# Kernel tuning notes

Hardware: AMD Instinct MI355X
Metric: run time of the kernel (lower is better)

The kernel has to match this reference:

```python
import jax, jax.numpy as jnp
import numpy as np
import math

N_HEAD = 16

def _rope_tables(seq, dh, dtype):
    inv_freq = 1.0 / (10000.0 ** (jnp.arange(0, dh, 2, dtype=jnp.float32) / dh))
    angle = jnp.arange(seq, dtype=jnp.float32)[:, None] * inv_freq[None, :]  # [S, dh/2]
    sin = jnp.repeat(jnp.sin(angle), 2, axis=-1).astype(dtype)  # [S, dh]
    cos = jnp.repeat(jnp.cos(angle), 2, axis=-1).astype(dtype)
    return sin, cos

def _rotate_half(x):
    x_even = x[..., ::2]
    x_odd = x[..., 1::2]
    return jnp.stack([-x_odd, x_even], axis=-1).reshape(x.shape)

def _apply_rope(x, sin, cos):
    # x: [B, H, S, dh]; sin/cos: [S, dh]
    return x * cos[None, None] + _rotate_half(x) * sin[None, None]

def setup_inputs() -> dict:
    key = jax.random.key(0)
    ks = jax.random.split(key, 9)
    B, S, D = 2, 2048, 2048
    scale = 1.0 / math.sqrt(D)
    x = jax.random.normal(ks[0], (B, S, D), dtype=jnp.float32)
    wq = jax.random.normal(ks[1], (D, D), dtype=jnp.float32) * scale
    wk = jax.random.normal(ks[2], (D, D), dtype=jnp.float32) * scale
    wv = jax.random.normal(ks[3], (D, D), dtype=jnp.float32) * scale
    wo = jax.random.normal(ks[4], (D, D), dtype=jnp.float32) * scale
    bq = jnp.zeros((D,), jnp.float32)
    bk = jnp.zeros((D,), jnp.float32)
    bv = jnp.zeros((D,), jnp.float32)
    bo = jnp.zeros((D,), jnp.float32)
    # causal mask: True = masked (strict upper triangle)
    mask = jnp.triu(jnp.ones((S, S), dtype=bool), k=1)[None, None]  # [1,1,S,S]
    return {"x": x, "wq": wq, "bq": bq, "wk": wk, "bk": bk, "wv": wv, "bv": bv,
            "wo": wo, "bo": bo, "mask": mask}

def reference(x, wq, bq, wk, bk, wv, bv, wo, bo, mask):
    B, S, D = x.shape
    H = N_HEAD
    dh = D // H
    # projections (torch Linear: x @ W.T + b)
    q = (x @ wq.T + bq).reshape(B, S, H, dh).transpose(0, 2, 1, 3)  # [B,H,S,dh]
    k = (x @ wk.T + bk).reshape(B, S, H, dh).transpose(0, 2, 1, 3)
    v = (x @ wv.T + bv).reshape(B, S, H, dh).transpose(0, 2, 1, 3)
    sin, cos = _rope_tables(S, dh, x.dtype)
    q = _apply_rope(q, sin, cos)
    k = _apply_rope(k, sin, cos)
    scores = jnp.einsum('bhqd,bhkd->bhqk', q, k) / math.sqrt(dh)
    scores = jnp.where(mask, -jnp.inf, scores)
    attn = jax.nn.softmax(scores, axis=-1)
    attn = jnp.nan_to_num(attn, nan=0.0)
    out = jnp.einsum('bhqk,bhkd->bhqd', attn, v)  # [B,H,S,dh]
    out = out.transpose(0, 2, 1, 3).reshape(B, S, D)
    return out @ wo.T + bo
```

## Files before the change

### kernel.cpp

```cpp
#include <hip/hip_runtime.h>
#include <math.h>


typedef _Float16 half8 __attribute__((ext_vector_type(8)));
typedef _Float16 half4v __attribute__((ext_vector_type(4)));
typedef float f32x4 __attribute__((ext_vector_type(4)));

__device__ __forceinline__ void gl_lds16(const void* g, void* l) {
  __builtin_amdgcn_global_load_lds(
      (const __attribute__((address_space(1))) unsigned int*)g,
      (__attribute__((address_space(3))) unsigned int*)l, 16, 0, 0);
}

__global__ void cast_f32_f16(const float* __restrict__ src, _Float16* __restrict__ dst, int n4) {
  int i = blockIdx.x * blockDim.x + threadIdx.x;
  if (i >= n4) return;
  float4 v = reinterpret_cast<const float4*>(src)[i];
  half4v o;
  o[0] = (_Float16)v.x; o[1] = (_Float16)v.y; o[2] = (_Float16)v.z; o[3] = (_Float16)v.w;
  reinterpret_cast<half4v*>(dst)[i] = o;
}

__global__ void cast_w(const float* __restrict__ w0, const float* __restrict__ w1,
                       const float* __restrict__ w2, const float* __restrict__ w3,
                       _Float16* __restrict__ wdst) {
  const float* s = blockIdx.y == 0 ? w0 : blockIdx.y == 1 ? w1 : blockIdx.y == 2 ? w2 : w3;
  int i = blockIdx.x * blockDim.x + threadIdx.x;
  float4 v = reinterpret_cast<const float4*>(s)[i];
  half4v o;
  o[0] = (_Float16)v.x; o[1] = (_Float16)v.y; o[2] = (_Float16)v.z; o[3] = (_Float16)v.w;
  reinterpret_cast<half4v*>(wdst)[(size_t)blockIdx.y * 1048576 + i] = o;
}

template <bool OUT_F32>
__global__ __launch_bounds__(512, 2) void gemm_bt256(
    const _Float16* __restrict__ A,
    const _Float16* __restrict__ B,
    const float* __restrict__ b0, const float* __restrict__ b1,
    const float* __restrict__ b2,
    void* __restrict__ Cout,
    int M, int N, int K) {
  __shared__ _Float16 As[2][16384];
  __shared__ _Float16 Bs[2][16384];
  const int bm = blockIdx.y * 256, bn = blockIdx.x * 256;
  const int tid = threadIdx.x;
  const int wave = tid >> 6, lane = tid & 63;
  const int quad = lane >> 4, l16 = lane & 15;
  const int wm = (wave >> 2) * 128, wn = (wave & 3) * 64;

  const int srow = tid >> 3;
  const int sx = (tid & 7) ^ (srow & 7);
  const _Float16* Ag = A + (size_t)(bm + srow) * K + sx * 8;
  const _Float16* Bg[4];
#pragma unroll
  for (int c = 0; c < 4; ++c) {
    int r = (((c * 2 + (srow >> 5)) & 3) << 6) + ((c >> 1) << 5) + (srow & 31);
    Bg[c] = B + (size_t)(bn + r) * K + sx * 8;
  }

#define STAGE_A(buf, R, kt) \
  gl_lds16(Ag + (size_t)(R) * K + (kt) * 64, &As[buf][(R) * 64 + tid * 8])
#define STAGE_B(buf, c, kt) \
  gl_lds16(Bg[c] + (kt) * 64, &Bs[buf][(c) * 4096 + tid * 8])

  const int axor = l16 & 7;
  const int sl0 = ((0 + quad) ^ axor) * 8;
  const int sl1 = ((4 + quad) ^ axor) * 8;
  const int aoff = (wm + l16) * 64;
  const int q4 = (wn >> 6) * 32;

#define RD_A(i, kk) \
  (*reinterpret_cast<const half8*>(&As[cur][aoff + (i) * 1024 + ((kk) ? sl1 : sl0)]))
#define RD_B(j, kk) \
  (*reinterpret_cast<const half8*>( \
      &Bs[cur][((((j) >> 1) * 128 + q4 + ((j) & 1) * 16 + l16)) * 64 + ((kk) ? sl1 : sl0)]))

  f32x4 acc[8][4];
#pragma unroll
  for (int i = 0; i < 8; ++i)
#pragma unroll
    for (int j = 0; j < 4; ++j) acc[i][j] = f32x4{0.f, 0.f, 0.f, 0.f};

  half8 a[4][2], b[4][2];
  const int NT = K >> 6;

  STAGE_A(0, 0, 0); STAGE_A(0, 128, 0);
  STAGE_B(0, 0, 0); STAGE_B(0, 1, 0);
  STAGE_B(0, 2, 0); STAGE_B(0, 3, 0);
  STAGE_A(0, 64, 0); STAGE_A(0, 192, 0);
  if (NT > 1) {
    STAGE_A(1, 0, 1); STAGE_A(1, 128, 1);
    STAGE_B(1, 0, 1); STAGE_B(1, 1, 1);
    STAGE_B(1, 2, 1); STAGE_B(1, 3, 1);
    asm volatile("s_waitcnt vmcnt(6)");
  } else {
    asm volatile("s_waitcnt vmcnt(0)");
  }
  __builtin_amdgcn_s_barrier();

  for (int t = 0; t < NT; ++t) {
    const int cur = t & 1, nxt = cur ^ 1;
    const bool pf1 = (t + 1 < NT);
    const bool pf2 = (t + 2 < NT);

#pragma unroll
    for (int i = 0; i < 4; ++i) {
      a[i][0] = RD_A(i, 0); a[i][1] = RD_A(i, 1);
    }
#pragma unroll
    for (int j = 0; j < 2; ++j) {
      b[j][0] = RD_B(j, 0); b[j][1] = RD_B(j, 1);
    }
    if (pf1) { STAGE_A(nxt, 64, t + 1); STAGE_A(nxt, 192, t + 1); }
    __builtin_amdgcn_s_barrier();
    __builtin_amdgcn_s_setprio(1);
#pragma unroll
    for (int i = 0; i < 4; ++i)
#pragma unroll
      for (int j = 0; j < 2; ++j) {
        acc[i][j] = __builtin_amdgcn_mfma_f32_16x16x32_f16(a[i][0], b[j][0], acc[i][j], 0, 0, 0);
        acc[i][j] = __builtin_amdgcn_mfma_f32_16x16x32_f16(a[i][1], b[j][1], acc[i][j], 0, 0, 0);
      }
    __builtin_amdgcn_s_setprio(0);
    __builtin_amdgcn_s_barrier();

#pragma unroll
    for (int j = 2; j < 4; ++j) {
      b[j][0] = RD_B(j, 0); b[j][1] = RD_B(j, 1);
    }
    if (pf2) { STAGE_A(cur, 0, t + 2); STAGE_A(cur, 128, t + 2); }
    __builtin_amdgcn_s_barrier();
    __builtin_amdgcn_s_setprio(1);
#pragma unroll
    for (int i = 0; i < 4; ++i)
#pragma unroll
      for (int j = 2; j < 4; ++j) {
        acc[i][j] = __builtin_amdgcn_mfma_f32_16x16x32_f16(a[i][0], b[j][0], acc[i][j], 0, 0, 0);
        acc[i][j] = __builtin_amdgcn_mfma_f32_16x16x32_f16(a[i][1], b[j][1], acc[i][j], 0, 0, 0);
      }
    __builtin_amdgcn_s_setprio(0);
    __builtin_amdgcn_s_barrier();

#pragma unroll
    for (int i = 0; i < 4; ++i) {
      a[i][0] = RD_A(i + 4, 0); a[i][1] = RD_A(i + 4, 1);
    }
    if (pf2) { STAGE_B(cur, 0, t + 2); STAGE_B(cur, 1, t + 2); }
    __builtin_amdgcn_s_barrier();
    __builtin_amdgcn_s_setprio(1);
#pragma unroll
    for (int i = 0; i < 4; ++i)
#pragma unroll
      for (int j = 0; j < 2; ++j) {
        acc[i + 4][j] = __builtin_amdgcn_mfma_f32_16x16x32_f16(a[i][0], b[j][0], acc[i + 4][j], 0, 0, 0);
        acc[i + 4][j] = __builtin_amdgcn_mfma_f32_16x16x32_f16(a[i][1], b[j][1], acc[i + 4][j], 0, 0, 0);
      }
    __builtin_amdgcn_s_setprio(0);
    __builtin_amdgcn_s_barrier();

    if (pf2) { STAGE_B(cur, 2, t + 2); STAGE_B(cur, 3, t + 2); }
    __builtin_amdgcn_s_barrier();
    __builtin_amdgcn_s_setprio(1);
#pragma unroll
    for (int i = 0; i < 4; ++i)
#pragma unroll
      for (int j = 2; j < 4; ++j) {
        acc[i + 4][j] = __builtin_amdgcn_mfma_f32_16x16x32_f16(a[i][0], b[j][0], acc[i + 4][j], 0, 0, 0);
        acc[i + 4][j] = __builtin_amdgcn_mfma_f32_16x16x32_f16(a[i][1], b[j][1], acc[i + 4][j], 0, 0, 0);
      }
    __builtin_amdgcn_s_setprio(0);
    if (pf2)
      asm volatile("s_waitcnt vmcnt(6)");
    else
      asm volatile("s_waitcnt vmcnt(0)");
    __builtin_amdgcn_s_barrier();
  }

#pragma unroll
  for (int j = 0; j < 4; ++j) {
    const int gc = bn + wn + j * 16 + l16;
    const float* bp = (gc < 2048) ? b0 : (gc < 4096 ? b1 : b2);
    const float bz = bp[gc & 2047];
#pragma unroll
    for (int i = 0; i < 8; ++i) {
#pragma unroll
      for (int r = 0; r < 4; ++r) {
        const int gr = bm + wm + i * 16 + quad * 4 + r;
        float v = acc[i][j][r] + bz;
        if (OUT_F32)
          reinterpret_cast<float*>(Cout)[(size_t)gr * N + gc] = v;
        else
          reinterpret_cast<_Float16*>(Cout)[(size_t)gr * N + gc] = (_Float16)v;
      }
    }
  }
#undef STAGE_A
#undef STAGE_B
#undef RD_A
#undef RD_B
}

__global__ void rope_inplace(_Float16* __restrict__ qkv, int ngroups) {
  int idx = blockIdx.x * blockDim.x + threadIdx.x;
  if (idx >= ngroups) return;
  int m = idx >> 8;
  int g = idx & 255;
  int s = m & 2047;
  const float scale = 0.088388347648318447f;
  size_t base = (size_t)m * 6144 + g * 8;
  half8 qv = *reinterpret_cast<const half8*>(qkv + base);
  half8 kv = *reinterpret_cast<const half8*>(qkv + base + 2048);
  half8 qo, ko;
#pragma unroll
  for (int j = 0; j < 4; ++j) {
    int i = (g * 4 + j) & 63;
    float ang = (float)s * exp2f(-0.2076205059304601f * (float)i);
    float sn, cs;
    __sincosf(ang, &sn, &cs);
    float e = (float)qv[j * 2], o = (float)qv[j * 2 + 1];
    qo[j * 2]     = (_Float16)((e * cs - o * sn) * scale);
    qo[j * 2 + 1] = (_Float16)((o * cs + e * sn) * scale);
    e = (float)kv[j * 2]; o = (float)kv[j * 2 + 1];
    ko[j * 2]     = (_Float16)(e * cs - o * sn);
    ko[j * 2 + 1] = (_Float16)(o * cs + e * sn);
  }
  *reinterpret_cast<half8*>(qkv + base) = qo;
  *reinterpret_cast<half8*>(qkv + base + 2048) = ko;
}

__global__ __launch_bounds__(256) void transpose_v(const _Float16* __restrict__ qkv,
                                                   _Float16* __restrict__ vt) {
  __shared__ _Float16 t[64][72];
  const int s0 = blockIdx.x * 64;
  const int d0 = blockIdx.y * 64;
  const int bh = blockIdx.z;
  const int b = bh >> 4, h = bh & 15;
  const int tid = threadIdx.x;
#pragma unroll
  for (int p = 0; p < 2; ++p) {
    int chunk = p * 256 + tid;
    int r = chunk >> 3, c8 = (chunk & 7) * 8;
    *reinterpret_cast<half8*>(&t[r][c8]) = *reinterpret_cast<const half8*>(
        &qkv[(size_t)(b * 2048 + s0 + r) * 6144 + 4096 + h * 128 + d0 + c8]);
  }
  __syncthreads();
#pragma unroll
  for (int p = 0; p < 2; ++p) {
    int chunk = p * 256 + tid;
    int dr = chunk >> 3, c8 = (chunk & 7) * 8;
    half8 o;
#pragma unroll
    for (int j = 0; j < 8; ++j) o[j] = t[c8 + j][dr];
    *reinterpret_cast<half8*>(&vt[(size_t)(bh * 128 + d0 + dr) * 2048 + s0 + c8]) = o;
  }
}

__global__ __launch_bounds__(256, 2) void attn_kernel(
    const _Float16* __restrict__ QKV,
    const _Float16* __restrict__ VT,
    _Float16* __restrict__ ctx) {
  constexpr int LD = 6144, S = 2048;
  __shared__ _Float16 Ks[2][8192];
  __shared__ _Float16 Vs[2][8192];
  __shared__ _Float16 P[4][16][80];
  const int bid = blockIdx.x;
  const int bh = bid & 31;
  const int qt = 31 - (bid >> 5);
  const int b = bh >> 4, h = bh & 15;
  const int tid = threadIdx.x;
  const int wv = tid >> 6, lane = tid & 63;
  const int quad = lane >> 4, l16 = lane & 15;
  const int q0 = qt * 64 + wv * 16;

  const _Float16* qp = QKV + (size_t)(b * S + q0 + l16) * LD + h * 128;
  half8 aq[4];
#pragma unroll
  for (int ks = 0; ks < 4; ++ks)
    aq[ks] = *reinterpret_cast<const half8*>(qp + ks * 32 + quad * 8);

  const _Float16* gk[4];
  const _Float16* gv[4];
  int lofs[4];
#pragma unroll
  for (int p = 0; p < 4; ++p) {
    int c = p * 256 + tid;
    int cs = c ^ ((c >> 3) & 7);
    int cl16 = cs & 15, cqd = (cs >> 4) & 3;
    int cks = (cs >> 6) & 3, cf = cs >> 8;
    gk[p] = QKV + (size_t)(b * S + cf * 16 + cl16) * LD + 2048 + h * 128 + cks * 32 + cqd * 8;
    int ckv = (cs >> 6) & 1, ct = cs >> 7;
    gv[p] = VT + (size_t)(bh * 128 + ct * 16 + cl16) * S + ckv * 32 + cqd * 8;
    lofs[p] = c * 8;
  }

  const int kofs = (l16 >> 3) * 64 + (((l16 & 7) ^ (quad * 2 + (l16 >> 3)))) * 8;

  f32x4 acc[8];
#pragma unroll
  for (int t = 0; t < 8; ++t) acc[t] = f32x4{0.f, 0.f, 0.f, 0.f};
  f32x4 lacc = f32x4{0.f, 0.f, 0.f, 0.f};

  half8 ones;
#pragma unroll
  for (int j = 0; j < 8; ++j) ones[j] = (_Float16)1.0f;

#pragma unroll
  for (int p = 0; p < 4; ++p) gl_lds16(gk[p], &Ks[0][lofs[p]]);
#pragma unroll
  for (int p = 0; p < 4; ++p) gl_lds16(gv[p], &Vs[0][lofs[p]]);

  for (int j = 0; j <= qt; ++j) {
    __syncthreads();
    const int cur = j & 1;
    if (j < qt) {
      const size_t ko = (size_t)(j + 1) * 64 * LD;
      const int vo = (j + 1) * 64;
#pragma unroll
      for (int p = 0; p < 4; ++p) gl_lds16(gk[p] + ko, &Ks[cur ^ 1][lofs[p]]);
#pragma unroll
      for (int p = 0; p < 4; ++p) gl_lds16(gv[p] + vo, &Vs[cur ^ 1][lofs[p]]);
    }
    f32x4 sf[4];
#pragma unroll
    for (int f = 0; f < 4; ++f) sf[f] = f32x4{0.f, 0.f, 0.f, 0.f};
#pragma unroll
    for (int f = 0; f < 4; ++f)
#pragma unroll
      for (int ks = 0; ks < 4; ++ks) {
        half8 bk = *reinterpret_cast<const half8*>(&Ks[cur][((f * 4 + ks) * 4 + quad) * 128 + kofs]);
        sf[f] = __builtin_amdgcn_mfma_f32_16x16x32_f16(aq[ks], bk, sf[f], 0, 0, 0);
      }
    if (j == qt) {
      const int key0 = j * 64;
#pragma unroll
      for (int f = 0; f < 4; ++f) {
        const int key = key0 + f * 16 + l16;
#pragma unroll
        for (int r = 0; r < 4; ++r) {
          const int row = q0 + quad * 4 + r;
          sf[f][r] = (key <= row) ? sf[f][r] : -1e30f;
        }
      }
    }
#pragma unroll
    for (int f = 0; f < 4; ++f)
#pragma unroll
      for (int r = 0; r < 4; ++r)
        P[wv][quad * 4 + r][f * 16 + l16] = (_Float16)__expf(sf[f][r] - 5.0f);
    half8 pa0 = *reinterpret_cast<const half8*>(&P[wv][l16][quad * 8]);
    half8 pa1 = *reinterpret_cast<const half8*>(&P[wv][l16][32 + quad * 8]);
#pragma unroll
    for (int t = 0; t < 8; ++t) {
      half8 bv0 = *reinterpret_cast<const half8*>(&Vs[cur][((t * 2 + 0) * 4 + quad) * 128 + kofs]);
      half8 bv1 = *reinterpret_cast<const half8*>(&Vs[cur][((t * 2 + 1) * 4 + quad) * 128 + kofs]);
      acc[t] = __builtin_amdgcn_mfma_f32_16x16x32_f16(pa0, bv0, acc[t], 0, 0, 0);
      acc[t] = __builtin_amdgcn_mfma_f32_16x16x32_f16(pa1, bv1, acc[t], 0, 0, 0);
    }
    lacc = __builtin_amdgcn_mfma_f32_16x16x32_f16(pa0, ones, lacc, 0, 0, 0);
    lacc = __builtin_amdgcn_mfma_f32_16x16x32_f16(pa1, ones, lacc, 0, 0, 0);
  }

  float inv[4];
#pragma unroll
  for (int r = 0; r < 4; ++r) inv[r] = 1.0f / lacc[r];
#pragma unroll
  for (int t = 0; t < 8; ++t)
#pragma unroll
    for (int r = 0; r < 4; ++r)
      ctx[(size_t)(b * S + q0 + quad * 4 + r) * 2048 + h * 128 + t * 16 + l16] =
          (_Float16)(acc[t][r] * inv[r]);
}

extern "C" void kernel_launch(void* const* d_in, const int* in_sizes, int n_in,
                              void* d_out, int out_size, void* d_ws, size_t ws_size,
                              hipStream_t stream) {
  const float* x  = (const float*)d_in[0];
  const float* wq = (const float*)d_in[1];
  const float* bq = (const float*)d_in[2];
  const float* wk = (const float*)d_in[3];
  const float* bk = (const float*)d_in[4];
  const float* wv = (const float*)d_in[5];
  const float* bv = (const float*)d_in[6];
  const float* wo = (const float*)d_in[7];
  const float* bo = (const float*)d_in[8];

  _Float16* W      = (_Float16*)d_ws;
  _Float16* xh     = W;
  _Float16* wqkvh  = xh + 8388608;
  _Float16* woh    = wqkvh + 12582912;
  _Float16* qkvlin = woh + 4194304;
  _Float16* vT     = xh;
  _Float16* ctx    = wqkvh;

  cast_f32_f16<<<8192, 256, 0, stream>>>(x, xh, 2097152);
  cast_w<<<dim3(4096, 4), 256, 0, stream>>>(wq, wk, wv, wo, wqkvh);

  gemm_bt256<false><<<dim3(24, 16), 512, 0, stream>>>(xh, wqkvh, bq, bk, bv, qkvlin,
                                                      4096, 6144, 2048);

  rope_inplace<<<4096, 256, 0, stream>>>(qkvlin, 1048576);
  transpose_v<<<dim3(32, 2, 32), 256, 0, stream>>>(qkvlin, vT);
  attn_kernel<<<1024, 256, 0, stream>>>(qkvlin, vT, ctx);

  gemm_bt256<true><<<dim3(8, 16), 512, 0, stream>>>(ctx, woh, bo, bo, bo, (float*)d_out,
                                                    4096, 2048, 2048);
}
```

Before: 439.5 us.

## Process two query tiles per attention block to reuse K/V loads

Each attention block now handles 128 query rows, split into two 64-row halves, and shares every K/V tile loaded into LDS between both halves. This halves the grid and the global-to-LDS traffic per query. It also orders blocks so that heavy and light causal tiles interleave. The cost is roughly twice the accumulator registers per thread, which may lower occupancy under the existing launch bounds, plus extra branching on the last tile.

```diff
diff --git a/kernel.cpp b/kernel.cpp
--- a/kernel.cpp
+++ b/kernel.cpp
@@ -265,18 +265,22 @@
   __shared__ _Float16 P[4][16][80];
   const int bid = blockIdx.x;
   const int bh = bid & 31;
-  const int qt = 31 - (bid >> 5);
+  const int idx = (bid >> 5) & 7;
+  const int qb = (bid >> 8) ? idx : 15 - idx;
   const int b = bh >> 4, h = bh & 15;
   const int tid = threadIdx.x;
   const int wv = tid >> 6, lane = tid & 63;
   const int quad = lane >> 4, l16 = lane & 15;
-  const int q0 = qt * 64 + wv * 16;
-
-  const _Float16* qp = QKV + (size_t)(b * S + q0 + l16) * LD + h * 128;
-  half8 aq[4];
-#pragma unroll
-  for (int ks = 0; ks < 4; ++ks)
-    aq[ks] = *reinterpret_cast<const half8*>(qp + ks * 32 + quad * 8);
+  const int q0 = qb * 128 + wv * 16;
+  const int NJ = 2 * qb + 2;
+
+  const _Float16* qp0 = QKV + (size_t)(b * S + q0 + l16) * LD + h * 128;
+  half8 aq0[4], aq1[4];
+#pragma unroll
+  for (int ks = 0; ks < 4; ++ks) {
+    aq0[ks] = *reinterpret_cast<const half8*>(qp0 + ks * 32 + quad * 8);
+    aq1[ks] = *reinterpret_cast<const half8*>(qp0 + (size_t)64 * LD + ks * 32 + quad * 8);
+  }
 
   const _Float16* gk[4];
   const _Float16* gv[4];
@@ -295,10 +299,14 @@
 
   const int kofs = (l16 >> 3) * 64 + (((l16 & 7) ^ (quad * 2 + (l16 >> 3)))) * 8;
 
-  f32x4 acc[8];
-#pragma unroll
-  for (int t = 0; t < 8; ++t) acc[t] = f32x4{0.f, 0.f, 0.f, 0.f};
-  f32x4 lacc = f32x4{0.f, 0.f, 0.f, 0.f};
+  f32x4 acc0[8], acc1[8];
+#pragma unroll
+  for (int t = 0; t < 8; ++t) {
+    acc0[t] = f32x4{0.f, 0.f, 0.f, 0.f};
+    acc1[t] = f32x4{0.f, 0.f, 0.f, 0.f};
+  }
+  f32x4 lacc0 = f32x4{0.f, 0.f, 0.f, 0.f};
+  f32x4 lacc1 = f32x4{0.f, 0.f, 0.f, 0.f};
 
   half8 ones;
 #pragma unroll
@@ -309,10 +317,10 @@
 #pragma unroll
   for (int p = 0; p < 4; ++p) gl_lds16(gv[p], &Vs[0][lofs[p]]);
 
-  for (int j = 0; j <= qt; ++j) {
+  for (int j = 0; j < NJ; ++j) {
     __syncthreads();
     const int cur = j & 1;
-    if (j < qt) {
+    if (j + 1 < NJ) {
       const size_t ko = (size_t)(j + 1) * 64 * LD;
       const int vo = (j + 1) * 64;
 #pragma unroll
@@ -320,55 +328,91 @@
 #pragma unroll
       for (int p = 0; p < 4; ++p) gl_lds16(gv[p] + vo, &Vs[cur ^ 1][lofs[p]]);
     }
-    f32x4 sf[4];
-#pragma unroll
-    for (int f = 0; f < 4; ++f) sf[f] = f32x4{0.f, 0.f, 0.f, 0.f};
+    const bool h0 = (j < NJ - 1);
+    f32x4 sf0[4], sf1[4];
+#pragma unroll
+    for (int f = 0; f < 4; ++f) {
+      sf0[f] = f32x4{0.f, 0.f, 0.f, 0.f};
+      sf1[f] = f32x4{0.f, 0.f, 0.f, 0.f};
+    }
 #pragma unroll
     for (int f = 0; f < 4; ++f)
 #pragma unroll
       for (int ks = 0; ks < 4; ++ks) {
         half8 bk = *reinterpret_cast<const half8*>(&Ks[cur][((f * 4 + ks) * 4 + quad) * 128 + kofs]);
-        sf[f] = __builtin_amdgcn_mfma_f32_16x16x32_f16(aq[ks], bk, sf[f], 0, 0, 0);
-      }
-    if (j == qt) {
-      const int key0 = j * 64;
+        sf0[f] = __builtin_amdgcn_mfma_f32_16x16x32_f16(aq0[ks], bk, sf0[f], 0, 0, 0);
+        sf1[f] = __builtin_amdgcn_mfma_f32_16x16x32_f16(aq1[ks], bk, sf1[f], 0, 0, 0);
+      }
+    if (j == NJ - 2) {
 #pragma unroll
       for (int f = 0; f < 4; ++f) {
-        const int key = key0 + f * 16 + l16;
-#pragma unroll
-        for (int r = 0; r < 4; ++r) {
-          const int row = q0 + quad * 4 + r;
-          sf[f][r] = (key <= row) ? sf[f][r] : -1e30f;
-        }
-      }
+        const int key = j * 64 + f * 16 + l16;
+#pragma unroll
+        for (int r = 0; r < 4; ++r)
+          sf0[f][r] = (key <= q0 + quad * 4 + r) ? sf0[f][r] : -1e30f;
+      }
+    }
+    if (j == NJ - 1) {
+#pragma unroll
+      for (int f = 0; f < 4; ++f) {
+        const int key = j * 64 + f * 16 + l16;
+#pragma unroll
+        for (int r = 0; r < 4; ++r)
+          sf1[f][r] = (key <= q0 + 64 + quad * 4 + r) ? sf1[f][r] : -1e30f;
+      }
+    }
+    half8 pa0a, pa0b, pa1a, pa1b;
+    if (h0) {
+#pragma unroll
+      for (int f = 0; f < 4; ++f)
+#pragma unroll
+        for (int r = 0; r < 4; ++r)
+          P[wv][quad * 4 + r][f * 16 + l16] = (_Float16)__expf(sf0[f][r] - 5.0f);
+      pa0a = *reinterpret_cast<const half8*>(&P[wv][l16][quad * 8]);
+      pa0b = *reinterpret_cast<const half8*>(&P[wv][l16][32 + quad * 8]);
     }
 #pragma unroll
     for (int f = 0; f < 4; ++f)
 #pragma unroll
       for (int r = 0; r < 4; ++r)
-        P[wv][quad * 4 + r][f * 16 + l16] = (_Float16)__expf(sf[f][r] - 5.0f);
-    half8 pa0 = *reinterpret_cast<const half8*>(&P[wv][l16][quad * 8]);
-    half8 pa1 = *reinterpret_cast<const half8*>(&P[wv][l16][32 + quad * 8]);
+        P[wv][quad * 4 + r][f * 16 + l16] = (_Float16)__expf(sf1[f][r] - 5.0f);
+    pa1a = *reinterpret_cast<const half8*>(&P[wv][l16][quad * 8]);
+    pa1b = *reinterpret_cast<const half8*>(&P[wv][l16][32 + quad * 8]);
 #pragma unroll
     for (int t = 0; t < 8; ++t) {
       half8 bv0 = *reinterpret_cast<const half8*>(&Vs[cur][((t * 2 + 0) * 4 + quad) * 128 + kofs]);
       half8 bv1 = *reinterpret_cast<const half8*>(&Vs[cur][((t * 2 + 1) * 4 + quad) * 128 + kofs]);
-      acc[t] = __builtin_amdgcn_mfma_f32_16x16x32_f16(pa0, bv0, acc[t], 0, 0, 0);
-      acc[t] = __builtin_amdgcn_mfma_f32_16x16x32_f16(pa1, bv1, acc[t], 0, 0, 0);
-    }
-    lacc = __builtin_amdgcn_mfma_f32_16x16x32_f16(pa0, ones, lacc, 0, 0, 0);
-    lacc = __builtin_amdgcn_mfma_f32_16x16x32_f16(pa1, ones, lacc, 0, 0, 0);
-  }
-
-  float inv[4];
-#pragma unroll
-  for (int r = 0; r < 4; ++r) inv[r] = 1.0f / lacc[r];
+      if (h0) {
+        acc0[t] = __builtin_amdgcn_mfma_f32_16x16x32_f16(pa0a, bv0, acc0[t], 0, 0, 0);
+        acc0[t] = __builtin_amdgcn_mfma_f32_16x16x32_f16(pa0b, bv1, acc0[t], 0, 0, 0);
+      }
+      acc1[t] = __builtin_amdgcn_mfma_f32_16x16x32_f16(pa1a, bv0, acc1[t], 0, 0, 0);
+      acc1[t] = __builtin_amdgcn_mfma_f32_16x16x32_f16(pa1b, bv1, acc1[t], 0, 0, 0);
+    }
+    if (h0) {
+      lacc0 = __builtin_amdgcn_mfma_f32_16x16x32_f16(pa0a, ones, lacc0, 0, 0, 0);
+      lacc0 = __builtin_amdgcn_mfma_f32_16x16x32_f16(pa0b, ones, lacc0, 0, 0, 0);
+    }
+    lacc1 = __builtin_amdgcn_mfma_f32_16x16x32_f16(pa1a, ones, lacc1, 0, 0, 0);
+    lacc1 = __builtin_amdgcn_mfma_f32_16x16x32_f16(pa1b, ones, lacc1, 0, 0, 0);
+  }
+
+  float inv0[4], inv1[4];
+#pragma unroll
+  for (int r = 0; r < 4; ++r) {
+    inv0[r] = 1.0f / lacc0[r];
+    inv1[r] = 1.0f / lacc1[r];
+  }
 #pragma unroll
   for (int t = 0; t < 8; ++t)
 #pragma unroll
-    for (int r = 0; r < 4; ++r)
-      ctx[(size_t)(b * S + q0 + quad * 4 + r) * 2048 + h * 128 + t * 16 + l16] =
-          (_Float16)(acc[t][r] * inv[r]);
+    for (int r = 0; r < 4; ++r) {
+      const int row0 = q0 + quad * 4 + r;
+      ctx[(size_t)(b * S + row0) * 2048 + h * 128 + t * 16 + l16] =
+          (_Float16)(acc0[t][r] * inv0[r]);
+      ctx[(size_t)(b * S + row0 + 64) * 2048 + h * 128 + t * 16 + l16] =
+          (_Float16)(acc1[t][r] * inv1[r]);
+    }
 }
 
 extern "C" void kernel_launch(void* const* d_in, const int* in_sizes, int n_in,
@@ -400,7 +444,7 @@
 
   rope_inplace<<<4096, 256, 0, stream>>>(qkvlin, 1048576);
   transpose_v<<<dim3(32, 2, 32), 256, 0, stream>>>(qkvlin, vT);
-  attn_kernel<<<1024, 256, 0, stream>>>(qkvlin, vT, ctx);
+  attn_kernel<<<512, 256, 0, stream>>>(qkvlin, vT, ctx);
 
   gemm_bt256<true><<<dim3(8, 16), 512, 0, stream>>>(ctx, woh, bo, bo, bo, (float*)d_out,
                                                     4096, 2048, 2048);
```

Result: no change. 438.8 us (-0.2%).
